# Kernel optimization log

Measured on AMD Instinct MI355X. Metric: run time of the kernel, lower is better.

The kernel has to match this reference:

```python
import jax, jax.numpy as jnp
from jax import lax
import numpy as np

BATCH = 524288
SEQ_LEN = 64


def setup_inputs() -> dict:
    key = jax.random.key(0)
    ka, kb = jax.random.split(key)
    a = jax.random.randint(ka, (BATCH, SEQ_LEN), 0, 10).astype(jnp.float32)
    b = jax.random.randint(kb, (BATCH, SEQ_LEN), 0, 10).astype(jnp.float32)
    # RNNCell params as hardcoded in Adder._initialize_weights
    weight_ih = jnp.array([[1.0, 1.0]], dtype=jnp.float32)   # (hidden=1, input=2)
    weight_hh = jnp.array([[1.0]], dtype=jnp.float32)        # (1, 1)
    bias_ih = jnp.zeros((1,), dtype=jnp.float32)
    bias_hh = jnp.zeros((1,), dtype=jnp.float32)
    return {"a": a, "b": b, "weight_ih": weight_ih, "weight_hh": weight_hh,
            "bias_ih": bias_ih, "bias_hh": bias_hh}


def reference(a, b, weight_ih, weight_hh, bias_ih, bias_hh):
    # a, b: (B, S) base-10 digits; carry h: (B, 1) hidden state.
    # Process digits from least significant (rightmost) to most significant.
    xs = jnp.stack([a, b], axis=-1)            # (B, S, 2)
    xs = jnp.flip(xs, axis=1)                  # reversed digit order
    xs = jnp.swapaxes(xs, 0, 1)                # (S, B, 2) for scan

    def step(h, x):
        # RNNCell with relu: u = relu(x @ W_ih^T + b_ih + h @ W_hh^T + b_hh)
        u = jax.nn.relu(x @ weight_ih.T + bias_ih + h @ weight_hh.T + bias_hh)  # (B,1)
        carry = jax.nn.relu(u - 9.0) - jax.nn.relu(u - 10.0)                    # (B,1)
        s = x[:, 0] + x[:, 1] + h[:, 0]                                         # (B,)
        digit = s - 10.0 * carry[:, 0]                                          # (B,)
        return carry, digit

    h0 = jnp.zeros((a.shape[0], 1), dtype=a.dtype)
    _, digits_rev = lax.scan(step, h0, xs)     # (S, B), least-significant first
    digits = jnp.flip(digits_rev, axis=0).T    # (B, S), original order
    return digits
```

## Files before the change

### kernel.cpp

```cpp
#include <hip/hip_runtime.h>


typedef float v4f __attribute__((ext_vector_type(4)));

__device__ __forceinline__ v4f add_tile(const v4f av, const v4f bv,
                                        const int k, const int pos) {
    const float s0 = av.x + bv.x;
    const float s1 = av.y + bv.y;
    const float s2 = av.z + bv.z;
    const float s3 = av.w + bv.w;

    float gc = (s3 >= 10.0f) ? 1.0f : 0.0f;
    gc = (s2 + gc >= 10.0f) ? 1.0f : 0.0f;
    gc = (s1 + gc >= 10.0f) ? 1.0f : 0.0f;
    gc = (s0 + gc >= 10.0f) ? 1.0f : 0.0f;
    const bool Gb = (gc != 0.0f);
    const bool Pb = (s0 == 9.0f) & (s1 == 9.0f) & (s2 == 9.0f) & (s3 == 9.0f);

    const unsigned long long g_mask = __ballot(Gb);
    const unsigned long long p_mask = __ballot(Pb);
    unsigned int g16 = (unsigned int)(g_mask >> (k * 16)) & 0xFFFFu;
    unsigned int p16 = (unsigned int)(p_mask >> (k * 16)) & 0xFFFFu;
    g16 = __brev(g16) >> 16;
    p16 = __brev(p16) >> 16;
    const unsigned int pg  = p16 | g16;
    const unsigned int c16 = (pg + g16) ^ pg ^ g16;
    const float cin = (float)((c16 >> pos) & 1u);

    const float u3 = s3 + cin; const float c3 = (u3 >= 10.0f) ? 1.0f : 0.0f;
    const float u2 = s2 + c3;  const float c2 = (u2 >= 10.0f) ? 1.0f : 0.0f;
    const float u1 = s1 + c2;  const float c1 = (u1 >= 10.0f) ? 1.0f : 0.0f;
    const float u0 = s0 + c1;  const float c0 = (u0 >= 10.0f) ? 1.0f : 0.0f;

    v4f dv;
    dv.x = u0 - 10.0f * c0;
    dv.y = u1 - 10.0f * c1;
    dv.z = u2 - 10.0f * c2;
    dv.w = u3 - 10.0f * c3;
    return dv;
}

__global__ __launch_bounds__(256) void adder_kernel(
    const v4f* __restrict__ a,
    const v4f* __restrict__ b,
    v4f* __restrict__ out,
    long long n_tiles)
{
    const int lane = (int)(threadIdx.x & 63);
    const int k    = lane >> 4;
    const int pos  = 15 - (lane & 15);

    const long long wave_id = (long long)blockIdx.x * 4 + (threadIdx.x >> 6);
    const long long t0 = wave_id * 4;
    if (t0 >= n_tiles) return;

    if (t0 + 4 <= n_tiles) {
        const long long i0 = t0 * 64 + lane;
        const v4f a0 = a[i0];
        const v4f b0 = b[i0];
        const v4f a1 = a[i0 + 64];
        const v4f b1 = b[i0 + 64];
        const v4f a2 = a[i0 + 128];
        const v4f b2 = b[i0 + 128];
        const v4f a3 = a[i0 + 192];
        const v4f b3 = b[i0 + 192];

        __builtin_nontemporal_store(add_tile(a0, b0, k, pos), &out[i0]);
        __builtin_nontemporal_store(add_tile(a1, b1, k, pos), &out[i0 + 64]);
        __builtin_nontemporal_store(add_tile(a2, b2, k, pos), &out[i0 + 128]);
        __builtin_nontemporal_store(add_tile(a3, b3, k, pos), &out[i0 + 192]);
    } else {
        for (long long t = t0; t < n_tiles; ++t) {
            const long long i = t * 64 + lane;
            __builtin_nontemporal_store(add_tile(a[i], b[i], k, pos), &out[i]);
        }
    }
}

extern "C" void kernel_launch(void* const* d_in, const int* in_sizes, int n_in,
                              void* d_out, int out_size, void* d_ws, size_t ws_size,
                              hipStream_t stream) {
    const v4f* a = (const v4f*)d_in[0];
    const v4f* b = (const v4f*)d_in[1];
    v4f* out = (v4f*)d_out;

    const long long n_rows  = (long long)in_sizes[0] / 64;
    const long long n_tiles = (n_rows + 3) / 4;
    const long long n_waves = (n_tiles + 3) / 4;
    const long long blocks  = (n_waves + 3) / 4;
    adder_kernel<<<(int)blocks, 256, 0, stream>>>(a, b, out, n_tiles);
}
```

Measured before the change: 321.1 us.

## Switch to grid-stride persistent loop with software-prefetched loads

```diff
diff --git a/kernel.cpp b/kernel.cpp
--- a/kernel.cpp
+++ b/kernel.cpp
@@ -44,37 +44,30 @@
     const v4f* __restrict__ a,
     const v4f* __restrict__ b,
     v4f* __restrict__ out,
-    long long n_tiles)
+    long long n_v4)
 {
     const int lane = (int)(threadIdx.x & 63);
     const int k    = lane >> 4;
     const int pos  = 15 - (lane & 15);
 
-    const long long wave_id = (long long)blockIdx.x * 4 + (threadIdx.x >> 6);
-    const long long t0 = wave_id * 4;
-    if (t0 >= n_tiles) return;
+    const long long base   = (long long)blockIdx.x * blockDim.x + threadIdx.x;
+    const long long stride = (long long)gridDim.x * blockDim.x;
 
-    if (t0 + 4 <= n_tiles) {
-        const long long i0 = t0 * 64 + lane;
-        const v4f a0 = a[i0];
-        const v4f b0 = b[i0];
-        const v4f a1 = a[i0 + 64];
-        const v4f b1 = b[i0 + 64];
-        const v4f a2 = a[i0 + 128];
-        const v4f b2 = b[i0 + 128];
-        const v4f a3 = a[i0 + 192];
-        const v4f b3 = b[i0 + 192];
+    if (base >= n_v4) return;
 
-        __builtin_nontemporal_store(add_tile(a0, b0, k, pos), &out[i0]);
-        __builtin_nontemporal_store(add_tile(a1, b1, k, pos), &out[i0 + 64]);
-        __builtin_nontemporal_store(add_tile(a2, b2, k, pos), &out[i0 + 128]);
-        __builtin_nontemporal_store(add_tile(a3, b3, k, pos), &out[i0 + 192]);
-    } else {
-        for (long long t = t0; t < n_tiles; ++t) {
-            const long long i = t * 64 + lane;
-            __builtin_nontemporal_store(add_tile(a[i], b[i], k, pos), &out[i]);
-        }
+    v4f ca = a[base];
+    v4f cb = b[base];
+    long long idx  = base;
+    long long next = base + stride;
+
+    while (next < n_v4) {
+        const v4f na = a[next];
+        const v4f nb = b[next];
+        out[idx] = add_tile(ca, cb, k, pos);
+        ca = na; cb = nb;
+        idx = next; next += stride;
     }
+    out[idx] = add_tile(ca, cb, k, pos);
 }
 
 extern "C" void kernel_launch(void* const* d_in, const int* in_sizes, int n_in,
@@ -84,9 +77,8 @@
     const v4f* b = (const v4f*)d_in[1];
     v4f* out = (v4f*)d_out;
 
-    const long long n_rows  = (long long)in_sizes[0] / 64;
-    const long long n_tiles = (n_rows + 3) / 4;
-    const long long n_waves = (n_tiles + 3) / 4;
-    const long long blocks  = (n_waves + 3) / 4;
-    adder_kernel<<<(int)blocks, 256, 0, stream>>>(a, b, out, n_tiles);
+    const long long n_rows = (long long)in_sizes[0] / 64;
+    const long long n_v4   = n_rows * 16;
+    const int blocks = 2048;
+    adder_kernel<<<blocks, 256, 0, stream>>>(a, b, out, n_v4);
 }
```

Result: faster. 314.5 us (-2.1%).
